# Kernel optimization log

Measured on AMD Instinct MI355X. Metric: run time of the kernel, lower is better.

## Reference

```python
import jax, jax.numpy as jnp
import numpy as np

EPS = 1e-7
N, L, BATCH = 512, 2, 128
N_IPF = 10


def setup_inputs() -> dict:
    key = jax.random.key(0)
    k1, k2, k3, k4 = jax.random.split(key, 4)
    return {
        "x": jax.random.randint(k1, (BATCH, N), 0, L, dtype=jnp.int32),
        "W": jax.random.normal(k2, (N, N), dtype=jnp.float32),
        "V_compress": jax.random.normal(k3, (N, L), dtype=jnp.float32),
        "E_compress": jax.random.normal(k4, (N, N, L, L), dtype=jnp.float32),
    }


def _moat_forward(W, V_compress, E_compress, x):
    n, l = V_compress.shape
    # marginals / joints
    V = jax.nn.softmax(V_compress, axis=1)              # (n, l)
    E = jnp.exp(E_compress)                              # (n, n, l, l)
    E = E / E.sum(axis=(-2, -1), keepdims=True)

    # 10-step Sinkhorn / IPF projection onto marginals V
    A_b = V[:, None, :, None]                            # (n, 1, l, 1)
    B_b = V[None, :, None, :]                            # (1, n, 1, l)
    for _ in range(N_IPF):
        row_marg = E.sum(axis=3, keepdims=True) + EPS    # (n, n, l, 1)
        col_marg = E.sum(axis=2, keepdims=True) + EPS    # (n, n, 1, l)
        E = E * (A_b / row_marg)
        E = E * (B_b / col_marg)
        E = E / (E.sum(axis=(-2, -1), keepdims=True) + EPS)

    # zero the diagonal (i == j) pairwise joints, clamp
    E = E * (1.0 - jnp.eye(n, dtype=E.dtype))[:, :, None, None]
    E = jnp.clip(E, 0.0, 1.0)

    # symmetric edge-weight matrix from strictly-lower-triangular sigmoid(W)
    Wm = jax.nn.sigmoid(W)
    Wm = jnp.tril(Wm, k=-1)
    Wm = Wm.T + Wm                                       # (n, n), zero diag
    L_0 = -Wm + jnp.diag(Wm.sum(axis=1))                 # graph Laplacian

    idx = jnp.arange(n)
    # Pr[b, i] = V[i, x[b, i]]
    Pr = V[idx[None, :], x]                              # (batch, n)
    # P[b, i, j] = E[i, j, x[b, i], x[b, j]]
    P = E[idx[None, :, None], idx[None, None, :], x[:, :, None], x[:, None, :]]  # (batch, n, n)
    P = P / (Pr[:, :, None] * Pr[:, None, :])

    WP = Wm[None, :, :] * P                              # (batch, n, n)
    Lb = -WP + jax.vmap(jnp.diag)(WP.sum(axis=2))        # batched Laplacian

    # matrix-tree theorem: logdet of the (n-1, n-1) principal minor
    _, logdet_L = jnp.linalg.slogdet(Lb[:, 1:, 1:])
    _, logdet_L0 = jnp.linalg.slogdet(L_0[1:, 1:])
    return jnp.log(Pr).sum(axis=1) + logdet_L - logdet_L0  # (batch,)


def reference(x, W, V_compress, E_compress):
    return _moat_forward(W, V_compress, E_compress, x)
```

## Files before the change

kernel.cpp:

```cpp
#include <hip/hip_runtime.h>
#include <hip/hip_bf16.h>
#include <math.h>

#define NDIM 512
#define NB   128
#define NMAT 129
#define EPSF 1e-7f
#define MS  ((size_t)262144)
#define LTS ((size_t)32768)
#define PSTR ((size_t)524288)

#define OFF_E   ((size_t)0)
#define OFF_WM  ((size_t)1048576)
#define OFF_V   ((size_t)(OFF_WM + 262144))
#define OFF_IPR ((size_t)(OFF_V + 1024))
#define OFF_LPR ((size_t)(OFF_IPR + 65536))
#define OFF_LD  ((size_t)(OFF_LPR + 128))
#define OFF_LT  ((size_t)1377792)
#define OFF_MAT ((size_t)(OFF_LT + (size_t)NMAT*LTS))

__global__ __launch_bounds__(256) void k_V(const float* __restrict__ Vc, float* __restrict__ V) {
  int i = blockIdx.x * 256 + threadIdx.x;
  if (i < NDIM) {
    float v0 = Vc[2*i], v1 = Vc[2*i+1];
    float mx = fmaxf(v0, v1);
    float e0 = expf(v0 - mx), e1 = expf(v1 - mx);
    float s = e0 + e1;
    V[2*i]   = e0 / s;
    V[2*i+1] = e1 / s;
  }
}

__global__ __launch_bounds__(256) void k_Wm(const float* __restrict__ W, float* __restrict__ Wm) {
  int idx = blockIdx.x * 256 + threadIdx.x;
  int i = idx >> 9, j = idx & 511;
  float v = 0.f;
  if (i > j)      v = 1.f / (1.f + expf(-W[i*NDIM + j]));
  else if (i < j) v = 1.f / (1.f + expf(-W[j*NDIM + i]));
  Wm[idx] = v;
}

__global__ __launch_bounds__(256) void k_E(const float* __restrict__ Ec, const float* __restrict__ V,
                                           float* __restrict__ E2) {
  int idx = blockIdx.x * 256 + threadIdx.x;
  int i = idx >> 9, j = idx & 511;
  float4 ec = reinterpret_cast<const float4*>(Ec)[idx];
  float e00 = expf(ec.x), e01 = expf(ec.y), e10 = expf(ec.z), e11 = expf(ec.w);
  float s = e00 + e01 + e10 + e11;
  float inv = 1.f / s;
  e00 *= inv; e01 *= inv; e10 *= inv; e11 *= inv;
  float A0 = V[2*i], A1 = V[2*i+1];
  float B0 = V[2*j], B1 = V[2*j+1];
  for (int t = 0; t < 10; ++t) {
    float rm0 = e00 + e01 + EPSF, rm1 = e10 + e11 + EPSF;
    float cm0 = e00 + e10 + EPSF, cm1 = e01 + e11 + EPSF;
    float f0 = A0 / rm0, f1 = A1 / rm1;
    e00 *= f0; e01 *= f0; e10 *= f1; e11 *= f1;
    float g0 = B0 / cm0, g1 = B1 / cm1;
    e00 *= g0; e10 *= g0; e01 *= g1; e11 *= g1;
    float ss = e00 + e01 + e10 + e11 + EPSF;
    float iv = 1.f / ss;
    e00 *= iv; e01 *= iv; e10 *= iv; e11 *= iv;
  }
  if (i == j) { e00 = 0.f; e01 = 0.f; e10 = 0.f; e11 = 0.f; }
  e00 = fminf(fmaxf(e00, 0.f), 1.f);
  e01 = fminf(fmaxf(e01, 0.f), 1.f);
  e10 = fminf(fmaxf(e10, 0.f), 1.f);
  e11 = fminf(fmaxf(e11, 0.f), 1.f);
  reinterpret_cast<float2*>(E2)[idx]               = make_float2(e00, e01);
  reinterpret_cast<float2*>(E2 + PSTR)[idx]        = make_float2(e10, e11);
}

__global__ __launch_bounds__(256) void k_Pr(const int* __restrict__ x, const float* __restrict__ V,
                                            float* __restrict__ invPr, float* __restrict__ logPr) {
  const int b = blockIdx.x;
  const int tid = threadIdx.x;
  float acc = 0.f;
  for (int ii = tid; ii < NDIM; ii += 256) {
    const int xv = x[b*NDIM + ii];
    const float p = V[2*ii + xv];
    invPr[b*NDIM + ii] = 1.f / p;
    acc += logf(p);
  }
  for (int off = 32; off > 0; off >>= 1) acc += __shfl_down(acc, off, 64);
  __shared__ float sw[4];
  if ((tid & 63) == 0) sw[tid >> 6] = acc;
  __syncthreads();
  if (tid == 0) logPr[b] = sw[0] + sw[1] + sw[2] + sw[3];
}

__global__ __launch_bounds__(512) void k_build(const int* __restrict__ x, const float* __restrict__ E2,
                                               const float* __restrict__ Wm, const float* __restrict__ invPr,
                                               float* __restrict__ Mall) {
  const int b = blockIdx.x;
  const int i = blockIdx.y*8 + (threadIdx.x >> 6);
  const int lane = threadIdx.x & 63;
  const int j0 = lane << 3;

  const float4 w0 = *(const float4*)(Wm + (size_t)i*NDIM + j0);
  const float4 w1 = *(const float4*)(Wm + (size_t)i*NDIM + j0 + 4);
  float wp[8];
  if (b < NB) {
    const int   xi   = x[b*NDIM + i];
    const float ipri = invPr[b*NDIM + i];
    const int4  xa = *(const int4*)(x + b*NDIM + j0);
    const int4  xb = *(const int4*)(x + b*NDIM + j0 + 4);
    const float4 pa = *(const float4*)(invPr + b*NDIM + j0);
    const float4 pb = *(const float4*)(invPr + b*NDIM + j0 + 4);
    const float* pl = E2 + (size_t)xi*PSTR + ((size_t)i*NDIM + j0)*2;
    const float4 ea = *(const float4*)(pl);
    const float4 eb = *(const float4*)(pl + 4);
    const float4 ec = *(const float4*)(pl + 8);
    const float4 ed = *(const float4*)(pl + 12);
    wp[0] = w0.x * (xa.x ? ea.y : ea.x) * pa.x;
    wp[1] = w0.y * (xa.y ? ea.w : ea.z) * pa.y;
    wp[2] = w0.z * (xa.z ? eb.y : eb.x) * pa.z;
    wp[3] = w0.w * (xa.w ? eb.w : eb.z) * pa.w;
    wp[4] = w1.x * (xb.x ? ec.y : ec.x) * pb.x;
    wp[5] = w1.y * (xb.y ? ec.w : ec.z) * pb.y;
    wp[6] = w1.z * (xb.z ? ed.y : ed.x) * pb.z;
    wp[7] = w1.w * (xb.w ? ed.w : ed.z) * pb.w;
    #pragma unroll
    for (int k = 0; k < 8; ++k) wp[k] *= ipri;
  } else {
    wp[0]=w0.x; wp[1]=w0.y; wp[2]=w0.z; wp[3]=w0.w;
    wp[4]=w1.x; wp[5]=w1.y; wp[6]=w1.z; wp[7]=w1.w;
  }
  float s = ((wp[0]+wp[1])+(wp[2]+wp[3])) + ((wp[4]+wp[5])+(wp[6]+wp[7]));
  #pragma unroll
  for (int off = 32; off > 0; off >>= 1) s += __shfl_xor(s, off, 64);

  float o[8];
  #pragma unroll
  for (int k = 0; k < 8; ++k) o[k] = -wp[k];
  if (i == 0) {
    #pragma unroll
    for (int k = 0; k < 8; ++k) o[k] = 0.f;
    if (lane == 0) o[0] = 1.f;
  } else {
    if (lane == 0) o[0] = 0.f;
    #pragma unroll
    for (int k = 0; k < 8; ++k)
      if (j0 + k == i) o[k] = s;
  }
  float* dst = Mall + (size_t)b*MS + (size_t)i*NDIM + j0;
  *(float4*)(dst)   = make_float4(o[0],o[1],o[2],o[3]);
  *(float4*)(dst+4) = make_float4(o[4],o[5],o[6],o[7]);
}

template<int KK>
struct PanelStep {
  static __device__ __forceinline__ void run(float (&a)[64], float (*pivrow)[72],
                                             int t, int m, float& logp) {
    float* pb = pivrow[KK & 1];
    if (t == KK) {
      #pragma unroll
      for (int c = 0; c < 16; ++c)
        *(float4*)(pb + c*4) = make_float4(a[c*4], a[c*4+1], a[c*4+2], a[c*4+3]);
      pb[64] = 1.0f / a[KK];
      logp += logf(fabsf(a[KK]));
    }
    __syncthreads();
    if (t > KK && t < m) {
      const float l = a[KK] * pb[64];
      a[KK] = l;
      #pragma unroll
      for (int c = KK + 1; c < 64; ++c)
        a[c] -= l * pb[c];
    }
    PanelStep<KK + 1>::run(a, pivrow, t, m, logp);
  }
};
template<>
struct PanelStep<64> {
  static __device__ __forceinline__ void run(float (&)[64], float (*)[72], int, int, float&) {}
};

__global__ __launch_bounds__(512) void k_panel(float* __restrict__ Mall, float* __restrict__ Lt,
                                               float* __restrict__ logdets, int k0, int mrem) {
  const int b = blockIdx.x;
  float* __restrict__ M = Mall + (size_t)b*MS;
  float* __restrict__ L = Lt + (size_t)b*LTS;
  const int t = threadIdx.x;
  const int m = NDIM - k0;
  __shared__ float pivrow[2][72];
  __shared__ float Ls[64][68];
  float a[64];
  if (t < m) {
    const float* row = M + (size_t)(k0+t)*NDIM + k0;
    #pragma unroll
    for (int c4 = 0; c4 < 16; ++c4) {
      float4 v = *(const float4*)(row + c4*4);
      a[c4*4+0]=v.x; a[c4*4+1]=v.y; a[c4*4+2]=v.z; a[c4*4+3]=v.w;
    }
  }
  float logp = 0.f;
  PanelStep<0>::run(a, pivrow, t, m, logp);
  if (t < m) {
    #pragma unroll
    for (int c = 0; c < 64; ++c) L[(size_t)c*NDIM + t] = a[c];
  }
  if (t < 64) {
    float v = logp;
    for (int off = 32; off > 0; off >>= 1) v += __shfl_down(v, off, 64);
    if (t == 0) logdets[b] = (k0 == 0) ? v : (logdets[b] + v);
    #pragma unroll
    for (int c = 0; c < 63; ++c)
      if (c < t) Ls[c][t] = a[c];
  }
  __syncthreads();
  if (t < mrem) {
    const int col = k0 + 64 + t;
    float u[64];
    #pragma unroll
    for (int r = 0; r < 64; ++r) u[r] = M[(size_t)(k0+r)*NDIM + col];
    #pragma unroll
    for (int p = 0; p < 63; ++p) {
      const float lv = u[p];
      #pragma unroll
      for (int kk = p+1; kk < 64; ++kk)
        u[kk] -= Ls[p][kk] * lv;
    }
    #pragma unroll
    for (int r = 1; r < 64; ++r) M[(size_t)(k0+r)*NDIM + col] = u[r];
  }
}

__global__ __launch_bounds__(256, 4) void k_gemm(float* __restrict__ Mall, const float* __restrict__ Lt,
                                                 int k0) {
  const int b = blockIdx.x;
  float* __restrict__ M = Mall + (size_t)b*MS;
  const float* __restrict__ L = Lt + (size_t)b*LTS;
  __shared__ float As[64][68];
  __shared__ float Bs[64][68];
  const int tid = threadIdx.x;
  const int tx = tid & 15, ty = tid >> 4;
  const int rowbase = 64 + blockIdx.y*64;
  const int colbase = 64 + blockIdx.z*64;
  #pragma unroll
  for (int i = 0; i < 4; ++i) {
    int q = tid + 256*i;
    int p = q >> 4, f = q & 15;
    *(float4*)&As[p][f*4] = *(const float4*)&L[(size_t)p*NDIM + rowbase + f*4];
    *(float4*)&Bs[p][f*4] = *(const float4*)&M[(size_t)(k0+p)*NDIM + (k0+colbase) + f*4];
  }
  float* Crow = M + (size_t)(k0+rowbase+ty*4)*NDIM + (k0+colbase+tx*4);
  float4 c0 = *(float4*)(Crow + 0*NDIM);
  float4 c1 = *(float4*)(Crow + 1*NDIM);
  float4 c2 = *(float4*)(Crow + 2*NDIM);
  float4 c3 = *(float4*)(Crow + 3*NDIM);
  __syncthreads();
  #pragma unroll
  for (int p = 0; p < 64; ++p) {
    const float4 av = *(const float4*)&As[p][ty*4];
    const float4 bv = *(const float4*)&Bs[p][tx*4];
    c0.x -= av.x*bv.x; c0.y -= av.x*bv.y; c0.z -= av.x*bv.z; c0.w -= av.x*bv.w;
    c1.x -= av.y*bv.x; c1.y -= av.y*bv.y; c1.z -= av.y*bv.z; c1.w -= av.y*bv.w;
    c2.x -= av.z*bv.x; c2.y -= av.z*bv.y; c2.z -= av.z*bv.z; c2.w -= av.z*bv.w;
    c3.x -= av.w*bv.x; c3.y -= av.w*bv.y; c3.z -= av.w*bv.z; c3.w -= av.w*bv.w;
  }
  *(float4*)(Crow + 0*NDIM) = c0;
  *(float4*)(Crow + 1*NDIM) = c1;
  *(float4*)(Crow + 2*NDIM) = c2;
  *(float4*)(Crow + 3*NDIM) = c3;
}

__global__ void k_final(const float* __restrict__ logPr, const float* __restrict__ logdets,
                        float* __restrict__ out) {
  int t = threadIdx.x;
  if (t < NB) out[t] = logPr[t] + logdets[t] - logdets[NB];
}

extern "C" void kernel_launch(void* const* d_in, const int* in_sizes, int n_in,
                              void* d_out, int out_size, void* d_ws, size_t ws_size,
                              hipStream_t stream) {
  const int*   x  = (const int*)  d_in[0];
  const float* W  = (const float*)d_in[1];
  const float* Vc = (const float*)d_in[2];
  const float* Ec = (const float*)d_in[3];
  float* out = (float*)d_out;
  float* ws  = (float*)d_ws;
  (void)in_sizes; (void)n_in; (void)out_size; (void)ws_size;

  float* Mat = ws + OFF_MAT;
  float* Lt  = ws + OFF_LT;
  float* Ld  = ws + OFF_LD;

  k_V  <<<2,    256, 0, stream>>>(Vc, ws + OFF_V);
  k_Wm <<<1024, 256, 0, stream>>>(W,  ws + OFF_WM);
  k_E  <<<1024, 256, 0, stream>>>(Ec, ws + OFF_V, ws + OFF_E);
  k_Pr <<<NB,   256, 0, stream>>>(x,  ws + OFF_V, ws + OFF_IPR, ws + OFF_LPR);
  dim3 gb(NMAT, 64);
  k_build<<<gb, 512, 0, stream>>>(x, ws + OFF_E, ws + OFF_WM, ws + OFF_IPR, Mat);

  for (int s = 0; s < 8; ++s) {
    const int k0 = s*64;
    const int mrem = NDIM - k0 - 64;
    k_panel<<<NMAT, 512, 0, stream>>>(Mat, Lt, Ld, k0, mrem);
    if (mrem > 0) {
      const int nt = mrem/64;
      dim3 gg(NMAT, nt, nt);
      k_gemm<<<gg, 256, 0, stream>>>(Mat, Lt, k0);
    }
  }
  k_final<<<1, 128, 0, stream>>>(ws + OFF_LPR, Ld, out);
}
```

Baseline: 697.5 us.

## Fuse blocked LU panel and trailing GEMM into one persistent kernel per matrix

Replaces the 15 alternating panel and GEMM launches with a single kernel in which one 512-thread block runs the whole blocked LU for its matrix. The panel factorisation, triangular solve and trailing updates all happen inside that block, synchronised with __syncthreads. This removes launch overhead and inter-kernel gaps. In exchange, the trailing update loses its per-tile grid parallelism: only 129 blocks run, each doing its GEMM tiles serially, so the GPU may be underused.

Result: slower. 1.227 ms (+75.9%).

```diff
diff --git a/kernel.cpp b/kernel.cpp
--- a/kernel.cpp
+++ b/kernel.cpp
@@ -176,93 +176,98 @@
   static __device__ __forceinline__ void run(float (&)[64], float (*)[72], int, int, float&) {}
 };
 
-__global__ __launch_bounds__(512) void k_panel(float* __restrict__ Mall, float* __restrict__ Lt,
-                                               float* __restrict__ logdets, int k0, int mrem) {
+__global__ __launch_bounds__(512) void k_LU(float* __restrict__ Mall, float* __restrict__ LtAll,
+                                            float* __restrict__ logdets) {
   const int b = blockIdx.x;
   float* __restrict__ M = Mall + (size_t)b*MS;
-  float* __restrict__ L = Lt + (size_t)b*LTS;
+  float* __restrict__ L = LtAll + (size_t)b*LTS;
   const int t = threadIdx.x;
-  const int m = NDIM - k0;
+  const int tx = t & 15, ty = t >> 4;
   __shared__ float pivrow[2][72];
-  __shared__ float Ls[64][68];
-  float a[64];
-  if (t < m) {
-    const float* row = M + (size_t)(k0+t)*NDIM + k0;
-    #pragma unroll
-    for (int c4 = 0; c4 < 16; ++c4) {
-      float4 v = *(const float4*)(row + c4*4);
-      a[c4*4+0]=v.x; a[c4*4+1]=v.y; a[c4*4+2]=v.z; a[c4*4+3]=v.w;
-    }
-  }
-  float logp = 0.f;
-  PanelStep<0>::run(a, pivrow, t, m, logp);
-  if (t < m) {
-    #pragma unroll
-    for (int c = 0; c < 64; ++c) L[(size_t)c*NDIM + t] = a[c];
-  }
-  if (t < 64) {
-    float v = logp;
-    for (int off = 32; off > 0; off >>= 1) v += __shfl_down(v, off, 64);
-    if (t == 0) logdets[b] = (k0 == 0) ? v : (logdets[b] + v);
-    #pragma unroll
-    for (int c = 0; c < 63; ++c)
-      if (c < t) Ls[c][t] = a[c];
-  }
-  __syncthreads();
-  if (t < mrem) {
-    const int col = k0 + 64 + t;
-    float u[64];
-    #pragma unroll
-    for (int r = 0; r < 64; ++r) u[r] = M[(size_t)(k0+r)*NDIM + col];
-    #pragma unroll
-    for (int p = 0; p < 63; ++p) {
-      const float lv = u[p];
-      #pragma unroll
-      for (int kk = p+1; kk < 64; ++kk)
-        u[kk] -= Ls[p][kk] * lv;
-    }
-    #pragma unroll
-    for (int r = 1; r < 64; ++r) M[(size_t)(k0+r)*NDIM + col] = u[r];
-  }
-}
-
-__global__ __launch_bounds__(256, 4) void k_gemm(float* __restrict__ Mall, const float* __restrict__ Lt,
-                                                 int k0) {
-  const int b = blockIdx.x;
-  float* __restrict__ M = Mall + (size_t)b*MS;
-  const float* __restrict__ L = Lt + (size_t)b*LTS;
+  __shared__ float Ls[64][72];
   __shared__ float As[64][68];
   __shared__ float Bs[64][68];
-  const int tid = threadIdx.x;
-  const int tx = tid & 15, ty = tid >> 4;
-  const int rowbase = 64 + blockIdx.y*64;
-  const int colbase = 64 + blockIdx.z*64;
-  #pragma unroll
-  for (int i = 0; i < 4; ++i) {
-    int q = tid + 256*i;
-    int p = q >> 4, f = q & 15;
-    *(float4*)&As[p][f*4] = *(const float4*)&L[(size_t)p*NDIM + rowbase + f*4];
-    *(float4*)&Bs[p][f*4] = *(const float4*)&M[(size_t)(k0+p)*NDIM + (k0+colbase) + f*4];
-  }
-  float* Crow = M + (size_t)(k0+rowbase+ty*4)*NDIM + (k0+colbase+tx*4);
-  float4 c0 = *(float4*)(Crow + 0*NDIM);
-  float4 c1 = *(float4*)(Crow + 1*NDIM);
-  float4 c2 = *(float4*)(Crow + 2*NDIM);
-  float4 c3 = *(float4*)(Crow + 3*NDIM);
-  __syncthreads();
-  #pragma unroll
-  for (int p = 0; p < 64; ++p) {
-    const float4 av = *(const float4*)&As[p][ty*4];
-    const float4 bv = *(const float4*)&Bs[p][tx*4];
-    c0.x -= av.x*bv.x; c0.y -= av.x*bv.y; c0.z -= av.x*bv.z; c0.w -= av.x*bv.w;
-    c1.x -= av.y*bv.x; c1.y -= av.y*bv.y; c1.z -= av.y*bv.z; c1.w -= av.y*bv.w;
-    c2.x -= av.z*bv.x; c2.y -= av.z*bv.y; c2.z -= av.z*bv.z; c2.w -= av.z*bv.w;
-    c3.x -= av.w*bv.x; c3.y -= av.w*bv.y; c3.z -= av.w*bv.z; c3.w -= av.w*bv.w;
-  }
-  *(float4*)(Crow + 0*NDIM) = c0;
-  *(float4*)(Crow + 1*NDIM) = c1;
-  *(float4*)(Crow + 2*NDIM) = c2;
-  *(float4*)(Crow + 3*NDIM) = c3;
+  float ldall = 0.f;
+
+  for (int s = 0; s < 8; ++s) {
+    const int k0 = s*64;
+    const int m = NDIM - k0;
+    const int mrem = m - 64;
+
+    float a[64];
+    if (t < m) {
+      const float* row = M + (size_t)(k0+t)*NDIM + k0;
+      #pragma unroll
+      for (int c4 = 0; c4 < 16; ++c4) {
+        float4 v = *(const float4*)(row + c4*4);
+        a[c4*4+0]=v.x; a[c4*4+1]=v.y; a[c4*4+2]=v.z; a[c4*4+3]=v.w;
+      }
+    }
+    float logp = 0.f;
+    PanelStep<0>::run(a, pivrow, t, m, logp);
+    if (t < m) {
+      #pragma unroll
+      for (int c = 0; c < 64; ++c) L[(size_t)c*NDIM + t] = a[c];
+    }
+    if (t < 64) {
+      #pragma unroll
+      for (int c = 0; c < 64; ++c) Ls[c][t] = a[c];
+      float v = logp;
+      for (int off = 32; off > 0; off >>= 1) v += __shfl_down(v, off, 64);
+      if (t == 0) ldall += v;
+    }
+    __syncthreads();
+
+    if (mrem > 0) {
+      if (t < mrem) {
+        const int col = k0 + 64 + t;
+        float u[64];
+        #pragma unroll
+        for (int r = 0; r < 64; ++r) u[r] = M[(size_t)(k0+r)*NDIM + col];
+        #pragma unroll
+        for (int p = 0; p < 63; ++p) {
+          const float lv = u[p];
+          #pragma unroll
+          for (int kk = p+1; kk < 64; ++kk)
+            u[kk] -= Ls[p][kk] * lv;
+        }
+        #pragma unroll
+        for (int r = 1; r < 64; ++r) M[(size_t)(k0+r)*NDIM + col] = u[r];
+      }
+      __syncthreads();
+
+      const int nt = mrem >> 6;
+      for (int ti = 0; ti < nt; ++ti) {
+        const int rowbase = 64 + ti*64;
+        for (int tj = 0; tj < nt; ++tj) {
+          const int colbase = 64 + tj*64;
+          float* Crow = M + (size_t)(k0+rowbase+ty*2)*NDIM + (k0+colbase+tx*4);
+          float4 c0 = *(float4*)(Crow);
+          float4 c1 = *(float4*)(Crow + NDIM);
+          __syncthreads();
+          #pragma unroll
+          for (int i2 = 0; i2 < 2; ++i2) {
+            int q = t + 512*i2;
+            int p = q >> 4, f = q & 15;
+            *(float4*)&As[p][f*4] = *(const float4*)&L[(size_t)p*NDIM + rowbase + f*4];
+            *(float4*)&Bs[p][f*4] = *(const float4*)&M[(size_t)(k0+p)*NDIM + (k0+colbase) + f*4];
+          }
+          __syncthreads();
+          #pragma unroll
+          for (int p = 0; p < 64; ++p) {
+            const float2 av = *(const float2*)&As[p][ty*2];
+            const float4 bv = *(const float4*)&Bs[p][tx*4];
+            c0.x -= av.x*bv.x; c0.y -= av.x*bv.y; c0.z -= av.x*bv.z; c0.w -= av.x*bv.w;
+            c1.x -= av.y*bv.x; c1.y -= av.y*bv.y; c1.z -= av.y*bv.z; c1.w -= av.y*bv.w;
+          }
+          *(float4*)(Crow)        = c0;
+          *(float4*)(Crow + NDIM) = c1;
+        }
+      }
+    }
+    __syncthreads();
+  }
+  if (t == 0) logdets[b] = ldall;
 }
 
 __global__ void k_final(const float* __restrict__ logPr, const float* __restrict__ logdets,
@@ -293,15 +298,7 @@
   dim3 gb(NMAT, 64);
   k_build<<<gb, 512, 0, stream>>>(x, ws + OFF_E, ws + OFF_WM, ws + OFF_IPR, Mat);
 
-  for (int s = 0; s < 8; ++s) {
-    const int k0 = s*64;
-    const int mrem = NDIM - k0 - 64;
-    k_panel<<<NMAT, 512, 0, stream>>>(Mat, Lt, Ld, k0, mrem);
-    if (mrem > 0) {
-      const int nt = mrem/64;
-      dim3 gg(NMAT, nt, nt);
-      k_gemm<<<gg, 256, 0, stream>>>(Mat, Lt, k0);
-    }
-  }
+  k_LU<<<NMAT, 512, 0, stream>>>(Mat, Lt, Ld);
+
   k_final<<<1, 128, 0, stream>>>(ws + OFF_LPR, Ld, out);
 }
```

## Factor the panel's diagonal block in one wavefront and solve remaining rows

Applied to the files above, without the earlier changes.

Rewrites the panel LU. The 64x64 diagonal block is now factored by a single wavefront, with pivot rows broadcast through readlane instead of shared memory plus one block-wide barrier per pivot. All other rows then compute their L entries with an independent triangular solve against the stored U block. This removes 64 __syncthreads per panel. In exchange it adds a serial per-thread forward solve, and the diagonal block is handled by only 64 lanes.

Result: faster. 628.1 us (-9.9%).

```diff
diff --git a/kernel.cpp b/kernel.cpp
--- a/kernel.cpp
+++ b/kernel.cpp
@@ -18,6 +18,10 @@
 #define OFF_LD  ((size_t)(OFF_LPR + 128))
 #define OFF_LT  ((size_t)1377792)
 #define OFF_MAT ((size_t)(OFF_LT + (size_t)NMAT*LTS))
+
+__device__ __forceinline__ float rdlane(float v, int l) {
+  return __uint_as_float((unsigned)__builtin_amdgcn_readlane((int)__float_as_uint(v), l));
+}
 
 __global__ __launch_bounds__(256) void k_V(const float* __restrict__ Vc, float* __restrict__ V) {
   int i = blockIdx.x * 256 + threadIdx.x;
@@ -149,31 +153,41 @@
 }
 
 template<int KK>
-struct PanelStep {
-  static __device__ __forceinline__ void run(float (&a)[64], float (*pivrow)[72],
-                                             int t, int m, float& logp) {
-    float* pb = pivrow[KK & 1];
-    if (t == KK) {
-      #pragma unroll
-      for (int c = 0; c < 16; ++c)
-        *(float4*)(pb + c*4) = make_float4(a[c*4], a[c*4+1], a[c*4+2], a[c*4+3]);
-      pb[64] = 1.0f / a[KK];
-      logp += logf(fabsf(a[KK]));
-    }
-    __syncthreads();
-    if (t > KK && t < m) {
-      const float l = a[KK] * pb[64];
+struct WFact {
+  static __device__ __forceinline__ void run(float (&a)[64], const int lane,
+                                             float& mypiv, float& myrec) {
+    const float piv = rdlane(a[KK], KK);
+    const float rec = 1.0f / piv;
+    if (lane == KK) { mypiv = piv; myrec = rec; }
+    if (lane > KK) {
+      const float l = a[KK] * rec;
       a[KK] = l;
       #pragma unroll
       for (int c = KK + 1; c < 64; ++c)
-        a[c] -= l * pb[c];
-    }
-    PanelStep<KK + 1>::run(a, pivrow, t, m, logp);
+        a[c] -= l * rdlane(a[c], KK);
+    }
+    WFact<KK + 1>::run(a, lane, mypiv, myrec);
   }
 };
 template<>
-struct PanelStep<64> {
-  static __device__ __forceinline__ void run(float (&)[64], float (*)[72], int, int, float&) {}
+struct WFact<64> {
+  static __device__ __forceinline__ void run(float (&)[64], int, float&, float&) {}
+};
+
+template<int C>
+struct SolveStep {
+  static __device__ __forceinline__ void run(float (&a)[64], const float (*T)[72]) {
+    float acc = a[C];
+    #pragma unroll
+    for (int p = 0; p < C; ++p)
+      acc -= a[p] * T[C][p];
+    a[C] = acc * T[C][66];
+    SolveStep<C + 1>::run(a, T);
+  }
+};
+template<>
+struct SolveStep<64> {
+  static __device__ __forceinline__ void run(float (&)[64], const float (*)[72]) {}
 };
 
 __global__ __launch_bounds__(512) void k_panel(float* __restrict__ Mall, float* __restrict__ Lt,
@@ -183,8 +197,8 @@
   float* __restrict__ L = Lt + (size_t)b*LTS;
   const int t = threadIdx.x;
   const int m = NDIM - k0;
-  __shared__ float pivrow[2][72];
-  __shared__ float Ls[64][68];
+  __shared__ float T[64][72];
+
   float a[64];
   if (t < m) {
     const float* row = M + (size_t)(k0+t)*NDIM + k0;
@@ -194,35 +208,41 @@
       a[c4*4+0]=v.x; a[c4*4+1]=v.y; a[c4*4+2]=v.z; a[c4*4+3]=v.w;
     }
   }
-  float logp = 0.f;
-  PanelStep<0>::run(a, pivrow, t, m, logp);
-  if (t < m) {
-    #pragma unroll
-    for (int c = 0; c < 64; ++c) L[(size_t)c*NDIM + t] = a[c];
-  }
+
   if (t < 64) {
-    float v = logp;
+    float mypiv = 1.f, myrec = 1.f;
+    WFact<0>::run(a, t, mypiv, myrec);
+    #pragma unroll
+    for (int c = 0; c < 64; ++c) T[c][t] = a[c];
+    T[t][66] = myrec;
+    float v = logf(fabsf(mypiv));
+    #pragma unroll
     for (int off = 32; off > 0; off >>= 1) v += __shfl_down(v, off, 64);
     if (t == 0) logdets[b] = (k0 == 0) ? v : (logdets[b] + v);
-    #pragma unroll
-    for (int c = 0; c < 63; ++c)
-      if (c < t) Ls[c][t] = a[c];
   }
   __syncthreads();
-  if (t < mrem) {
-    const int col = k0 + 64 + t;
-    float u[64];
-    #pragma unroll
-    for (int r = 0; r < 64; ++r) u[r] = M[(size_t)(k0+r)*NDIM + col];
-    #pragma unroll
-    for (int p = 0; p < 63; ++p) {
-      const float lv = u[p];
-      #pragma unroll
-      for (int kk = p+1; kk < 64; ++kk)
-        u[kk] -= Ls[p][kk] * lv;
-    }
-    #pragma unroll
-    for (int r = 1; r < 64; ++r) M[(size_t)(k0+r)*NDIM + col] = u[r];
+
+  if (mrem > 0) {
+    if (t >= 64 && t < m) {
+      SolveStep<0>::run(a, T);
+      #pragma unroll
+      for (int c = 0; c < 64; ++c) L[(size_t)c*NDIM + t] = a[c];
+    }
+    if (t < mrem) {
+      const int col = k0 + 64 + t;
+      float u[64];
+      #pragma unroll
+      for (int r = 0; r < 64; ++r) u[r] = M[(size_t)(k0+r)*NDIM + col];
+      #pragma unroll
+      for (int p = 0; p < 63; ++p) {
+        const float lv = u[p];
+        #pragma unroll
+        for (int kk = p+1; kk < 64; ++kk)
+          u[kk] -= T[p][kk] * lv;
+      }
+      #pragma unroll
+      for (int r = 1; r < 64; ++r) M[(size_t)(k0+r)*NDIM + col] = u[r];
+    }
   }
 }
 
```
